# Kernel tuning notes

Hardware: AMD Instinct MI355X
Metric: run time of the kernel (lower is better)

The kernel has to match this reference:

```python
import jax, jax.numpy as jnp
import numpy as np

NUM_HEADS = 16

def setup_inputs() -> dict:
    key = jax.random.key(0)
    k1, k2, k3 = jax.random.split(key, 3)
    B, T, D = 4, 2048, 1024
    x = jax.random.normal(k1, (B, T, D), dtype=jnp.float32)
    # lecun_normal: std = 1/sqrt(fan_in)
    w = jax.random.normal(k2, (3 * D, D), dtype=jnp.float32) * (1.0 / np.sqrt(D))
    w_out = jax.random.normal(k3, (D, D), dtype=jnp.float32) * (1.0 / np.sqrt(D))
    return {"x": x, "w": w, "w_out": w_out}


def reference(x, w, w_out):
    B, T, D = x.shape
    H = NUM_HEADS
    L = D // H
    # qkv projection: (B,T,3D)
    q, k, v = jnp.split(jnp.matmul(x, w.T), 3, axis=2)
    # -> (T,B,H,L) time-major for the scan
    q = q.reshape(B, T, H, L).transpose(1, 0, 2, 3)
    k = k.reshape(B, T, H, L).transpose(1, 0, 2, 3)
    v = v.reshape(B, T, H, L).transpose(1, 0, 2, 3)
    scale = jax.lax.rsqrt(jnp.float32(L))
    k_exp = jnp.exp(k * scale) + 1e-6            # (T,B,H,L)
    k_norm = jnp.cumsum(k_exp, axis=0)           # causal normalizer
    qs = jax.nn.softmax(q * scale, axis=-1) / k_norm

    def step(carry, args):
        qs_t, k_t, v_t = args                    # each (B,H,L)
        # accumulate outer product k_t v_t^T into (B,H,L,L) state
        carry = carry + k_t[..., :, None] * v_t[..., None, :]
        y_t = jnp.einsum('bhl,bhlm->bhm', qs_t, carry)
        return carry, y_t

    init = jnp.zeros((B, H, L, L), dtype=x.dtype)
    _, y = jax.lax.scan(step, init, (qs, k_exp, v))   # y: (T,B,H,L)
    y = y.reshape(T, B, D).transpose(1, 0, 2)         # (B,T,D)
    return jnp.matmul(y, w_out)                       # Dense, no bias
```

## Files before the change

kernel.cpp:

```cpp
#include <hip/hip_runtime.h>
#include <math.h>

#define Bsz   4
#define Tsz   2048
#define Dsz   1024
#define Hsz   16
#define Lsz   64
#define BHsz  64
#define CH    64
#define NCH   32
#define QKVLD 3072
#define SCL   0.125f
#define QSC   512.0f
#define QSCI  (1.0f/512.0f)

typedef float  floatx4 __attribute__((ext_vector_type(4)));
typedef _Float16 half8 __attribute__((ext_vector_type(8)));
typedef _Float16 half4 __attribute__((ext_vector_type(4)));
typedef _Float16 half2v __attribute__((ext_vector_type(2)));

#define AS1 __attribute__((address_space(1)))
#define AS3 __attribute__((address_space(3)))

static __device__ __forceinline__ void gload_lds16(const void* g, void* l) {
  __builtin_amdgcn_global_load_lds((const AS1 unsigned int*)g,
                                   (AS3 unsigned int*)l, 16, 0, 0);
}

static __device__ __forceinline__ float wave_max64(float v) {
#pragma unroll
  for (int off = 1; off < 64; off <<= 1) v = fmaxf(v, __shfl_xor(v, off));
  return v;
}
static __device__ __forceinline__ float wave_sum64(float v) {
#pragma unroll
  for (int off = 1; off < 64; off <<= 1) v += __shfl_xor(v, off);
  return v;
}

__launch_bounds__(256)
__global__ void prep(const float* __restrict__ x, _Float16* __restrict__ xh,
                     const float* __restrict__ w, _Float16* __restrict__ wh,
                     const float* __restrict__ wo, _Float16* __restrict__ woT) {
  const int blk = blockIdx.x, tid = threadIdx.x;
  if (blk < 11264) {
    const float* in  = (blk < 8192) ? x : w;
    _Float16*   outp = (blk < 8192) ? xh : wh;
    const int bi = (blk < 8192) ? blk : blk - 8192;
    const int i = (bi * 256 + tid) * 4;
    float4 v = *(const float4*)(in + i);
    half4 h = { (_Float16)v.x, (_Float16)v.y, (_Float16)v.z, (_Float16)v.w };
    *(half4*)(outp + i) = h;
  } else {
    __shared__ float tile[32][33];
    const int bi = blk - 11264;
    const int bx = (bi & 31) * 32;
    const int by = (bi >> 5) * 32;
    const int tx = tid & 31, ty0 = tid >> 5;
#pragma unroll
    for (int p = 0; p < 4; p++) {
      const int ty = ty0 + p * 8;
      tile[ty][tx] = wo[(size_t)(by + ty) * 1024 + bx + tx];
    }
    __syncthreads();
#pragma unroll
    for (int p = 0; p < 4; p++) {
      const int ty = ty0 + p * 8;
      woT[(size_t)(bx + ty) * 1024 + by + tx] = (_Float16)tile[tx][ty];
    }
  }
}

__launch_bounds__(512, 2)
__global__ void qkv_gemm8(const _Float16* __restrict__ A, const _Float16* __restrict__ B,
                          _Float16* __restrict__ C) {
  __shared__ __align__(16) _Float16 AsF[2 * 256 * 64];
  __shared__ __align__(16) _Float16 BsF[2 * 256 * 64];
  const int tid  = threadIdx.x;
  const int wv   = tid >> 6, lane = tid & 63;
  const int wm   = wv >> 2, wn = wv & 3;
  const int fr   = lane & 15, fq = lane >> 4;

  const int flat = blockIdx.x;
  const int g  = (flat & 7) * 48 + (flat >> 3);
  const int m0 = (g / 12) * 256;
  const int n0 = (g % 12) * 256;

  const int srow = lane >> 3;
  const int scg  = (lane & 7) ^ srow;
  const int wv8  = wv * 8;
  const _Float16* aSrc = A + (size_t)(m0 + wv8 + srow) * 1024 + scg * 8;
  const _Float16* bSrc = B + (size_t)(n0 + wv8 + srow) * 1024 + scg * 8;

  const int sw  = fr & 7;
  const int ck0 = ((0 + fq) ^ sw) * 8;
  const int ck1 = ((4 + fq) ^ sw) * 8;
  const _Float16* apt = AsF + (wm * 64 + fr) * 64;
  const _Float16* bpt = BsF + (wn * 32 + fr) * 64;

  floatx4 acc[8][4];
#pragma unroll
  for (int i = 0; i < 8; i++)
#pragma unroll
    for (int j = 0; j < 4; j++) acc[i][j] = (floatx4){0.f, 0.f, 0.f, 0.f};

  half8 aF[8];
  half8 bF0[4], bF1[4];

#define BAR2() do { __builtin_amdgcn_s_barrier();                              \
                    asm volatile("" ::: "memory"); } while (0)
#define VMW4() asm volatile("s_waitcnt vmcnt(4)" ::: "memory")
#define SYNC() do { __builtin_amdgcn_s_barrier();                              \
    asm volatile("s_waitcnt lgkmcnt(0)" ::: "memory");                         \
    __builtin_amdgcn_sched_barrier(0); } while (0)

#define STAGE_A(kt, hm, sbuf) do {                                             \
    const _Float16* s_ = aSrc + (hm) * (128 * 1024) + (kt) * 64;               \
    gload_lds16(s_,             &AsF[(sbuf) * 16384 + ((hm) * 128 + wv8) * 64]);      \
    gload_lds16(s_ + 64 * 1024, &AsF[(sbuf) * 16384 + ((hm) * 128 + 64 + wv8) * 64]); \
  } while (0)
#define STAGE_B(kt, hm, sbuf) do {                                             \
    const _Float16* s_ = bSrc + (hm) * (128 * 1024) + (kt) * 64;               \
    gload_lds16(s_,             &BsF[(sbuf) * 16384 + ((hm) * 128 + wv8) * 64]);      \
    gload_lds16(s_ + 64 * 1024, &BsF[(sbuf) * 16384 + ((hm) * 128 + 64 + wv8) * 64]); \
  } while (0)

#define RD_A(buf, qm) do {                                                     \
    _Pragma("unroll")                                                          \
    for (int mf = 0; mf < 4; mf++) {                                           \
      const _Float16* p_ = apt + (buf) * 16384 + (qm) * 8192 + mf * 1024;      \
      aF[mf * 2]     = *(const half8*)(p_ + ck0);                              \
      aF[mf * 2 + 1] = *(const half8*)(p_ + ck1);                              \
    } } while (0)
#define RD_B(buf, qn, dst) do {                                                \
    _Pragma("unroll")                                                          \
    for (int nf = 0; nf < 2; nf++) {                                           \
      const _Float16* p_ = bpt + (buf) * 16384 + (qn) * 8192 + nf * 1024;      \
      dst[nf * 2]     = *(const half8*)(p_ + ck0);                             \
      dst[nf * 2 + 1] = *(const half8*)(p_ + ck1);                             \
    } } while (0)

#define MM(qm, qn, bb) do {                                                    \
    __builtin_amdgcn_s_setprio(1);                                             \
    _Pragma("unroll")                                                          \
    for (int mf = 0; mf < 4; mf++)                                             \
      _Pragma("unroll")                                                        \
      for (int nf = 0; nf < 2; nf++) {                                         \
        acc[(qm) * 4 + mf][(qn) * 2 + nf] = __builtin_amdgcn_mfma_f32_16x16x32_f16( \
            aF[mf * 2], bb[nf * 2], acc[(qm) * 4 + mf][(qn) * 2 + nf], 0, 0, 0);     \
        acc[(qm) * 4 + mf][(qn) * 2 + nf] = __builtin_amdgcn_mfma_f32_16x16x32_f16( \
            aF[mf * 2 + 1], bb[nf * 2 + 1], acc[(qm) * 4 + mf][(qn) * 2 + nf], 0, 0, 0); \
      }                                                                        \
    __builtin_amdgcn_s_setprio(0);                                             \
  } while (0)

  STAGE_A(0, 0, 0); STAGE_B(0, 0, 0); STAGE_A(0, 1, 0); STAGE_B(0, 1, 0);
  STAGE_A(1, 0, 1); STAGE_B(1, 0, 1);
  VMW4(); BAR2();

#pragma unroll 1
  for (int t = 0; t < 16; t += 2) {
    RD_A(0, 0); RD_B(0, 0, bF0); STAGE_A(t + 1, 1, 1);
    SYNC(); MM(0, 0, bF0); BAR2();

    RD_B(0, 1, bF1); STAGE_B(t + 1, 1, 1); STAGE_A(t + 2, 0, 0);
    SYNC(); MM(0, 1, bF1); BAR2();

    RD_A(0, 1); STAGE_B(t + 2, 0, 0);
    SYNC(); MM(1, 1, bF1); BAR2();

    VMW4();
    SYNC(); MM(1, 0, bF0); BAR2();

    RD_A(1, 0); RD_B(1, 0, bF0); STAGE_A(t + 2, 1, 0);
    SYNC(); MM(0, 0, bF0); BAR2();

    RD_B(1, 1, bF1); STAGE_B(t + 2, 1, 0); STAGE_A(t + 3, 0, 1);
    SYNC(); MM(0, 1, bF1); BAR2();

    RD_A(1, 1); STAGE_B(t + 3, 0, 1);
    SYNC(); MM(1, 1, bF1); BAR2();

    VMW4();
    SYNC(); MM(1, 0, bF0); BAR2();
  }

#undef MM
#undef RD_B
#undef RD_A
#undef STAGE_B
#undef STAGE_A
#undef SYNC
#undef VMW4
#undef BAR2

  const bool kreg = (n0 >= 1024) && (n0 < 2048);
#pragma unroll
  for (int qm = 0; qm < 2; qm++)
#pragma unroll
    for (int mf = 0; mf < 4; mf++) {
      const int row = m0 + qm * 128 + wm * 64 + mf * 16 + fq * 4;
#pragma unroll
      for (int qn = 0; qn < 2; qn++)
#pragma unroll
        for (int nf = 0; nf < 2; nf++) {
          const int col = n0 + qn * 128 + wn * 32 + nf * 16 + fr;
#pragma unroll
          for (int r = 0; r < 4; r++) {
            float v = acc[qm * 4 + mf][qn * 2 + nf][r];
            if (kreg) v = __expf(v * SCL) + 1e-6f;
            C[(size_t)(row + r) * 3072 + col] = (_Float16)v;
          }
        }
    }
}

__launch_bounds__(256)
__global__ void gemm_f16_bt_f32(const _Float16* __restrict__ A, const _Float16* __restrict__ B,
                                float* __restrict__ C, int M, int N, int K) {
  __shared__ _Float16 As[128][32];
  __shared__ _Float16 Bs[128][32];
  const int tid  = threadIdx.x;
  const int wave = tid >> 6, lane = tid & 63;
  const int flat = blockIdx.y * gridDim.x + blockIdx.x;
  const int xcd = flat & 7, g = flat >> 3;
  const int m0 = (xcd * 8 + (g & 7)) * 128;
  const int n0 = (g >> 3) * 128;
  const int wm = (wave >> 1) * 64, wn = (wave & 1) * 64;
  const int fr = lane & 15;
  const int fq = lane >> 4;
  const int lr = lane >> 2;
  const int lk = (lane & 3) * 8;

  floatx4 zero = {0.f, 0.f, 0.f, 0.f};
  floatx4 acc[4][4];
#pragma unroll
  for (int mt = 0; mt < 4; mt++)
#pragma unroll
    for (int nt = 0; nt < 4; nt++) acc[mt][nt] = zero;

  for (int k0 = 0; k0 < K; k0 += 32) {
    __syncthreads();
#pragma unroll
    for (int j = 0; j < 2; j++) {
      const int ia = wave * 2 + j;
      gload_lds16(A + (size_t)(m0 + ia * 16 + lr) * K + k0 + lk, &As[ia * 16][0]);
      gload_lds16(B + (size_t)(n0 + ia * 16 + lr) * K + k0 + lk, &Bs[ia * 16][0]);
    }
    __syncthreads();

    half8 af[4], bf[4];
#pragma unroll
    for (int i = 0; i < 4; i++) {
      af[i] = *(const half8*)&As[wm + i * 16 + fr][fq * 8];
      bf[i] = *(const half8*)&Bs[wn + i * 16 + fr][fq * 8];
    }
#pragma unroll
    for (int mt = 0; mt < 4; mt++)
#pragma unroll
      for (int nt = 0; nt < 4; nt++)
        acc[mt][nt] = __builtin_amdgcn_mfma_f32_16x16x32_f16(af[mt], bf[nt], acc[mt][nt], 0, 0, 0);
  }
#pragma unroll
  for (int mt = 0; mt < 4; mt++)
#pragma unroll
    for (int nt = 0; nt < 4; nt++)
#pragma unroll
      for (int r = 0; r < 4; r++) {
        const int row = m0 + wm + mt * 16 + fq * 4 + r;
        const int col = n0 + wn + nt * 16 + fr;
        C[(size_t)row * N + col] = acc[mt][nt][r];
      }
}

__launch_bounds__(256)
__global__ void chunk_kv(const _Float16* __restrict__ qkv, float* __restrict__ KV,
                         float* __restrict__ Ksum) {
  const int blk = blockIdx.x;
  const int bh = blk >> 3, cgrp = blk & 7;
  const int b = bh >> 4, h = bh & 15;
  const int tid = threadIdx.x;
  const int wave = tid >> 6, lane = tid & 63;
  const int fr = lane & 15, fq = lane >> 4;
  const int m2  = (tid & 31) * 2;
  const int tg8 = (tid >> 5) * 8;

  __shared__ __align__(16) _Float16 KxT[64][72];
  __shared__ __align__(16) _Float16 VT [64][72];

  for (int cc = 0; cc < 4; cc++) {
    const int c = cgrp * 4 + cc;
    const size_t base = ((size_t)(b * Tsz + c * CH)) * QKVLD + h * 64;
    __syncthreads();
    half8 klo, khi, vlo, vhi;
#pragma unroll
    for (int j = 0; j < 8; j++) {
      const int t = tg8 + j;
      half2v kk = *(const half2v*)(qkv + base + (size_t)t * QKVLD + 1024 + m2);
      klo[j] = kk[0]; khi[j] = kk[1];
      half2v vv = *(const half2v*)(qkv + base + (size_t)t * QKVLD + 2048 + m2);
      vlo[j] = vv[0]; vhi[j] = vv[1];
    }
    *(half8*)&KxT[m2][tg8]     = klo;
    *(half8*)&KxT[m2 + 1][tg8] = khi;
    *(half8*)&VT[m2][tg8]      = vlo;
    *(half8*)&VT[m2 + 1][tg8]  = vhi;
    __syncthreads();

    floatx4 acc[4];
#pragma unroll
    for (int j = 0; j < 4; j++) acc[j] = (floatx4){0.f, 0.f, 0.f, 0.f};
#pragma unroll
    for (int ks = 0; ks < 2; ks++) {
      half8 av = *(const half8*)&VT[wave * 16 + fr][ks * 32 + fq * 8];
#pragma unroll
      for (int j = 0; j < 4; j++) {
        half8 bv = *(const half8*)&KxT[j * 16 + fr][ks * 32 + fq * 8];
        acc[j] = __builtin_amdgcn_mfma_f32_16x16x32_f16(av, bv, acc[j], 0, 0, 0);
      }
    }
    float* KVp = KV + ((size_t)(bh * NCH + c)) * 4096;
#pragma unroll
    for (int j = 0; j < 4; j++)
#pragma unroll
      for (int r = 0; r < 4; r++)
        KVp[(wave * 16 + fq * 4 + r) * 64 + j * 16 + fr] = acc[j][r];

    if (tid < 64) {
      float s = 0.f;
      const half8* row = (const half8*)&KxT[tid][0];
#pragma unroll
      for (int j8 = 0; j8 < 8; j8++) {
        half8 v8 = row[j8];
#pragma unroll
        for (int j = 0; j < 8; j++) s += (float)v8[j];
      }
      Ksum[(bh * NCH + c) * 64 + tid] = s;
    }
  }
}

__launch_bounds__(256)
__global__ void prefix_kern(float* __restrict__ KV, float* __restrict__ Ksum) {
  const int tid = threadIdx.x;
  if (blockIdx.x < 256) {
    const int bh = blockIdx.x >> 2;
    const int e  = (blockIdx.x & 3) * 1024 + tid * 4;
    float4* p = (float4*)(KV + (size_t)bh * NCH * 4096 + e);
    float4 acc = {0.f, 0.f, 0.f, 0.f};
#pragma unroll 4
    for (int c = 0; c < NCH; c++) {
      float4 t = p[(size_t)c * 1024];
      p[(size_t)c * 1024] = acc;
      acc.x += t.x; acc.y += t.y; acc.z += t.z; acc.w += t.w;
    }
  } else {
    const int cid = (blockIdx.x - 256) * 256 + tid;
    const int bh = cid >> 4, l4 = cid & 15;
    float4* p = (float4*)(Ksum + (size_t)bh * NCH * 64) + l4;
    float4 acc = {0.f, 0.f, 0.f, 0.f};
#pragma unroll 4
    for (int c = 0; c < NCH; c++) {
      float4 t = p[c * 16];
      p[c * 16] = acc;
      acc.x += t.x; acc.y += t.y; acc.z += t.z; acc.w += t.w;
    }
  }
}

__launch_bounds__(256)
__global__ void chunk_y(const _Float16* __restrict__ qkv, const float* __restrict__ KV,
                        const float* __restrict__ Ksum, _Float16* __restrict__ Y) {
  const int bh = blockIdx.x, c = blockIdx.y;
  const int b = bh >> 4, h = bh & 15;
  const int tid = threadIdx.x;
  const int wave = tid >> 6, lane = tid & 63;
  const int fr = lane & 15, fq = lane >> 4;

  __shared__ __align__(16) _Float16 kxh[64][72];
  __shared__ __align__(16) _Float16 kxT[64][72];
  __shared__ __align__(16) _Float16 Ph[64][136];
  __shared__ __align__(16) _Float16 Bh[64][136];

  const size_t base = ((size_t)(b * Tsz + c * CH)) * QKVLD + h * 64;
  const float* KVp = KV + ((size_t)(bh * NCH + c)) * 4096;
  const int ksoff = (bh * NCH + c) * 64;

  _Float16 qreg[16];
#pragma unroll
  for (int i = 0; i < 16; i++)
    qreg[i] = qkv[base + (size_t)(wave * 16 + i) * QKVLD + lane];

  float ksb[4];
#pragma unroll
  for (int j = 0; j < 4; j++) ksb[j] = Ksum[ksoff + j * 16 + fr];

  {
    const int rr  = tid >> 3;
    const int sg8 = (tid & 7) * 8;
#pragma unroll
    for (int p = 0; p < 2; p++) {
      const int t = p * 32 + rr;
      *(half8*)&kxh[t][sg8] =
          *(const half8*)(qkv + base + (size_t)t * QKVLD + 1024 + sg8);
      *(half8*)&Ph[t][64 + sg8] =
          *(const half8*)(qkv + base + (size_t)t * QKVLD + 2048 + sg8);
    }
  }
  {
    const int m  = tid >> 2;
    const int l0 = (tid & 3) * 16;
#pragma unroll
    for (int q = 0; q < 2; q++) {
      float4 s0 = *(const float4*)(KVp + m * 64 + l0 + q * 8);
      float4 s1 = *(const float4*)(KVp + m * 64 + l0 + q * 8 + 4);
      half8 hh = { (_Float16)s0.x, (_Float16)s0.y, (_Float16)s0.z, (_Float16)s0.w,
                   (_Float16)s1.x, (_Float16)s1.y, (_Float16)s1.z, (_Float16)s1.w };
      *(half8*)&Bh[m][l0 + q * 8] = hh;
    }
  }
  __syncthreads();

  {
    const int l2  = (tid & 31) * 2;
    const int tg8 = (tid >> 5) * 8;
    half8 k0, k1, v0, v1;
#pragma unroll
    for (int j = 0; j < 8; j++) {
      const int t = tg8 + j;
      half2v kk = *(const half2v*)&kxh[t][l2];
      k0[j] = kk[0]; k1[j] = kk[1];
      half2v vv = *(const half2v*)&Ph[t][64 + l2];
      v0[j] = vv[0]; v1[j] = vv[1];
    }
    *(half8*)&kxT[l2][tg8]          = k0;
    *(half8*)&kxT[l2 + 1][tg8]      = k1;
    *(half8*)&Bh[l2][64 + tg8]      = v0;
    *(half8*)&Bh[l2 + 1][64 + tg8]  = v1;
  }
  __syncthreads();

  {
    floatx4 kacc[4];
#pragma unroll
    for (int j = 0; j < 4; j++) kacc[j] = (floatx4){0.f, 0.f, 0.f, 0.f};
#pragma unroll
    for (int ks = 0; ks < 2; ks++) {
      half8 af;
#pragma unroll
      for (int j = 0; j < 8; j++)
        af[j] = (ks * 32 + fq * 8 + j) <= (wave * 16 + fr) ? (_Float16)1.0f
                                                           : (_Float16)0.0f;
#pragma unroll
      for (int j = 0; j < 4; j++) {
        half8 bf = *(const half8*)&kxT[j * 16 + fr][ks * 32 + fq * 8];
        kacc[j] = __builtin_amdgcn_mfma_f32_16x16x32_f16(af, bf, kacc[j], 0, 0, 0);
      }
    }
    __syncthreads();
#pragma unroll
    for (int j = 0; j < 4; j++)
#pragma unroll
      for (int r = 0; r < 4; r++)
        kxT[wave * 16 + fq * 4 + r][j * 16 + fr] =
            (_Float16)(QSC / (ksb[j] + kacc[j][r]));
  }

#pragma unroll
  for (int i = 0; i < 16; i++) {
    const int t = wave * 16 + i;
    float v = (float)qreg[i] * SCL;
    float m = wave_max64(v);
    float e = __expf(v - m);
    float s = wave_sum64(e);
    Ph[t][lane] = (_Float16)((e / s) * (float)kxT[t][lane]);
  }
  __syncthreads();

  const int wm = (wave >> 1) * 32, wn = (wave & 1) * 32;
  {
    floatx4 a2[2][2];
#pragma unroll
    for (int mt = 0; mt < 2; mt++)
#pragma unroll
      for (int nt = 0; nt < 2; nt++) a2[mt][nt] = (floatx4){0.f, 0.f, 0.f, 0.f};
#pragma unroll
    for (int ks = 0; ks < 2; ks++) {
      half8 af[2], bf[2];
#pragma unroll
      for (int i = 0; i < 2; i++) {
        af[i] = *(const half8*)&Ph[wm + i * 16 + fr][ks * 32 + fq * 8];
        bf[i] = *(const half8*)&kxh[wn + i * 16 + fr][ks * 32 + fq * 8];
      }
#pragma unroll
      for (int mt = 0; mt < 2; mt++)
#pragma unroll
        for (int nt = 0; nt < 2; nt++)
          a2[mt][nt] = __builtin_amdgcn_mfma_f32_16x16x32_f16(af[mt], bf[nt], a2[mt][nt], 0, 0, 0);
    }
#pragma unroll
    for (int mt = 0; mt < 2; mt++)
#pragma unroll
      for (int nt = 0; nt < 2; nt++)
#pragma unroll
        for (int r = 0; r < 4; r++) {
          const int t = wm + mt * 16 + fq * 4 + r;
          const int s = wn + nt * 16 + fr;
          Ph[t][64 + s] = (_Float16)(s <= t ? a2[mt][nt][r] : 0.f);
        }
  }
  __syncthreads();

  {
    floatx4 acc[2][2];
#pragma unroll
    for (int mt = 0; mt < 2; mt++)
#pragma unroll
      for (int nt = 0; nt < 2; nt++) acc[mt][nt] = (floatx4){0.f, 0.f, 0.f, 0.f};
#pragma unroll
    for (int ks = 0; ks < 4; ks++) {
      half8 af[2], bf[2];
#pragma unroll
      for (int i = 0; i < 2; i++) {
        af[i] = *(const half8*)&Ph[wm + i * 16 + fr][ks * 32 + fq * 8];
        bf[i] = *(const half8*)&Bh[wn + i * 16 + fr][ks * 32 + fq * 8];
      }
#pragma unroll
      for (int mt = 0; mt < 2; mt++)
#pragma unroll
        for (int nt = 0; nt < 2; nt++)
          acc[mt][nt] = __builtin_amdgcn_mfma_f32_16x16x32_f16(af[mt], bf[nt], acc[mt][nt], 0, 0, 0);
    }
#pragma unroll
    for (int mt = 0; mt < 2; mt++)
#pragma unroll
      for (int nt = 0; nt < 2; nt++)
#pragma unroll
        for (int r = 0; r < 4; r++)
          kxh[wm + mt * 16 + fq * 4 + r][wn + nt * 16 + fr] =
              (_Float16)(acc[mt][nt][r] * QSCI);
  }
  __syncthreads();

  {
    const int ty = tid >> 2, sg = (tid & 3) * 16;
    _Float16* yrow = Y + (size_t)(b * Tsz + c * CH + ty) * Dsz + h * 64 + sg;
    *(half8*)(yrow)     = *(const half8*)&kxh[ty][sg];
    *(half8*)(yrow + 8) = *(const half8*)&kxh[ty][sg + 8];
  }
}

extern "C" void kernel_launch(void* const* d_in, const int* in_sizes, int n_in,
                              void* d_out, int out_size, void* d_ws, size_t ws_size,
                              hipStream_t stream) {
  const float* x     = (const float*)d_in[0];
  const float* w     = (const float*)d_in[1];
  const float* w_out = (const float*)d_in[2];
  float* out = (float*)d_out;

  _Float16* xh   = (_Float16*)d_ws;
  _Float16* Yh   = xh;
  _Float16* wh   = xh + (size_t)8192 * 1024;
  _Float16* woT  = wh + (size_t)3072 * 1024;
  _Float16* qkvh = woT + (size_t)1024 * 1024;
  float* KV   = (float*)(qkvh + (size_t)8192 * 3072);
  float* Ksum = KV + (size_t)BHsz * NCH * 4096;

  prep<<<12288, 256, 0, stream>>>(x, xh, w, wh, w_out, woT);

  qkv_gemm8<<<384, 512, 0, stream>>>(xh, wh, qkvh);

  chunk_kv<<<512, 256, 0, stream>>>(qkvh, KV, Ksum);
  prefix_kern<<<260, 256, 0, stream>>>(KV, Ksum);
  chunk_y<<<dim3(BHsz, NCH), 256, 0, stream>>>(qkvh, KV, Ksum, Yh);

  gemm_f16_bt_f32<<<dim3(8, 64), 256, 0, stream>>>(Yh, woT, out, 8192, 1024, 1024);
}
```

Before: 249.1 us.

## Fuse per-chunk KV state computation with the chunk prefix scan

```diff
diff --git a/kernel.cpp b/kernel.cpp
--- a/kernel.cpp
+++ b/kernel.cpp
@@ -274,98 +274,98 @@
 }
 
 __launch_bounds__(256)
-__global__ void chunk_kv(const _Float16* __restrict__ qkv, float* __restrict__ KV,
-                         float* __restrict__ Ksum) {
+__global__ void chunk_scan(const _Float16* __restrict__ qkv, float* __restrict__ KV,
+                           float* __restrict__ Ksum) {
   const int blk = blockIdx.x;
-  const int bh = blk >> 3, cgrp = blk & 7;
+  const int bh = blk >> 2, mq = blk & 3;
   const int b = bh >> 4, h = bh & 15;
   const int tid = threadIdx.x;
   const int wave = tid >> 6, lane = tid & 63;
   const int fr = lane & 15, fq = lane >> 4;
+
   const int m2  = (tid & 31) * 2;
   const int tg8 = (tid >> 5) * 8;
-
-  __shared__ __align__(16) _Float16 KxT[64][72];
-  __shared__ __align__(16) _Float16 VT [64][72];
-
-  for (int cc = 0; cc < 4; cc++) {
-    const int c = cgrp * 4 + cc;
-    const size_t base = ((size_t)(b * Tsz + c * CH)) * QKVLD + h * 64;
-    __syncthreads();
-    half8 klo, khi, vlo, vhi;
-#pragma unroll
-    for (int j = 0; j < 8; j++) {
-      const int t = tg8 + j;
-      half2v kk = *(const half2v*)(qkv + base + (size_t)t * QKVLD + 1024 + m2);
-      klo[j] = kk[0]; khi[j] = kk[1];
-      half2v vv = *(const half2v*)(qkv + base + (size_t)t * QKVLD + 2048 + m2);
-      vlo[j] = vv[0]; vhi[j] = vv[1];
-    }
-    *(half8*)&KxT[m2][tg8]     = klo;
-    *(half8*)&KxT[m2 + 1][tg8] = khi;
-    *(half8*)&VT[m2][tg8]      = vlo;
-    *(half8*)&VT[m2 + 1][tg8]  = vhi;
-    __syncthreads();
-
-    floatx4 acc[4];
-#pragma unroll
-    for (int j = 0; j < 4; j++) acc[j] = (floatx4){0.f, 0.f, 0.f, 0.f};
+  const int vcp2 = (tid & 7) * 2;
+  const int vtg8 = ((tid >> 3) & 7) * 8;
+
+  __shared__ __align__(16) _Float16 KxT[2][64][72];
+  __shared__ __align__(16) _Float16 VT [2][16][72];
+
+  const size_t bbase = ((size_t)b * Tsz) * QKVLD + h * 64;
+
+  half8 klo, khi, vlo, vhi;
+
+#define LOADC(c) do {                                                          \
+    const size_t base_ = bbase + (size_t)(c) * CH * QKVLD;                     \
+    _Pragma("unroll")                                                          \
+    for (int j = 0; j < 8; j++) {                                              \
+      half2v kk = *(const half2v*)(qkv + base_ + (size_t)(tg8 + j) * QKVLD + 1024 + m2); \
+      klo[j] = kk[0]; khi[j] = kk[1];                                          \
+    }                                                                          \
+    if (tid < 64) {                                                            \
+      _Pragma("unroll")                                                        \
+      for (int j = 0; j < 8; j++) {                                            \
+        half2v vv = *(const half2v*)(qkv + base_ + (size_t)(vtg8 + j) * QKVLD + 2048 + mq * 16 + vcp2); \
+        vlo[j] = vv[0]; vhi[j] = vv[1];                                        \
+      }                                                                        \
+    } } while (0)
+
+#define WRITEC(bufi) do {                                                      \
+    *(half8*)&KxT[bufi][m2][tg8]     = klo;                                    \
+    *(half8*)&KxT[bufi][m2 + 1][tg8] = khi;                                    \
+    if (tid < 64) {                                                            \
+      *(half8*)&VT[bufi][vcp2][vtg8]     = vlo;                                \
+      *(half8*)&VT[bufi][vcp2 + 1][vtg8] = vhi;                                \
+    } } while (0)
+
+  LOADC(0);
+  WRITEC(0);
+  __syncthreads();
+
+  floatx4 run = {0.f, 0.f, 0.f, 0.f};
+  float run_ks = 0.f;
+  int cur = 0;
+
+#pragma unroll 1
+  for (int c = 0; c < NCH; c++) {
+    if (c + 1 < NCH) LOADC(c + 1);
+
+    floatx4 acc = {0.f, 0.f, 0.f, 0.f};
 #pragma unroll
     for (int ks = 0; ks < 2; ks++) {
-      half8 av = *(const half8*)&VT[wave * 16 + fr][ks * 32 + fq * 8];
-#pragma unroll
-      for (int j = 0; j < 4; j++) {
-        half8 bv = *(const half8*)&KxT[j * 16 + fr][ks * 32 + fq * 8];
-        acc[j] = __builtin_amdgcn_mfma_f32_16x16x32_f16(av, bv, acc[j], 0, 0, 0);
-      }
-    }
+      half8 av = *(const half8*)&VT[cur][fr][ks * 32 + fq * 8];
+      half8 bv = *(const half8*)&KxT[cur][wave * 16 + fr][ks * 32 + fq * 8];
+      acc = __builtin_amdgcn_mfma_f32_16x16x32_f16(av, bv, acc, 0, 0, 0);
+    }
+
     float* KVp = KV + ((size_t)(bh * NCH + c)) * 4096;
 #pragma unroll
-    for (int j = 0; j < 4; j++)
-#pragma unroll
-      for (int r = 0; r < 4; r++)
-        KVp[(wave * 16 + fq * 4 + r) * 64 + j * 16 + fr] = acc[j][r];
-
-    if (tid < 64) {
+    for (int r = 0; r < 4; r++)
+      KVp[(mq * 16 + fq * 4 + r) * 64 + wave * 16 + fr] = run[r];
+    run = run + acc;
+
+    if (mq == 0 && tid < 64) {
       float s = 0.f;
-      const half8* row = (const half8*)&KxT[tid][0];
+      const half8* row = (const half8*)&KxT[cur][tid][0];
 #pragma unroll
       for (int j8 = 0; j8 < 8; j8++) {
         half8 v8 = row[j8];
 #pragma unroll
         for (int j = 0; j < 8; j++) s += (float)v8[j];
       }
-      Ksum[(bh * NCH + c) * 64 + tid] = s;
-    }
-  }
-}
-
-__launch_bounds__(256)
-__global__ void prefix_kern(float* __restrict__ KV, float* __restrict__ Ksum) {
-  const int tid = threadIdx.x;
-  if (blockIdx.x < 256) {
-    const int bh = blockIdx.x >> 2;
-    const int e  = (blockIdx.x & 3) * 1024 + tid * 4;
-    float4* p = (float4*)(KV + (size_t)bh * NCH * 4096 + e);
-    float4 acc = {0.f, 0.f, 0.f, 0.f};
-#pragma unroll 4
-    for (int c = 0; c < NCH; c++) {
-      float4 t = p[(size_t)c * 1024];
-      p[(size_t)c * 1024] = acc;
-      acc.x += t.x; acc.y += t.y; acc.z += t.z; acc.w += t.w;
-    }
-  } else {
-    const int cid = (blockIdx.x - 256) * 256 + tid;
-    const int bh = cid >> 4, l4 = cid & 15;
-    float4* p = (float4*)(Ksum + (size_t)bh * NCH * 64) + l4;
-    float4 acc = {0.f, 0.f, 0.f, 0.f};
-#pragma unroll 4
-    for (int c = 0; c < NCH; c++) {
-      float4 t = p[c * 16];
-      p[c * 16] = acc;
-      acc.x += t.x; acc.y += t.y; acc.z += t.z; acc.w += t.w;
-    }
-  }
+      Ksum[(bh * NCH + c) * 64 + tid] = run_ks;
+      run_ks += s;
+    }
+
+    if (c + 1 < NCH) {
+      WRITEC(cur ^ 1);
+      cur ^= 1;
+    }
+    __syncthreads();
+  }
+
+#undef WRITEC
+#undef LOADC
 }
 
 __launch_bounds__(256)
@@ -570,8 +570,7 @@
 
   qkv_gemm8<<<384, 512, 0, stream>>>(xh, wh, qkvh);
 
-  chunk_kv<<<512, 256, 0, stream>>>(qkvh, KV, Ksum);
-  prefix_kern<<<260, 256, 0, stream>>>(KV, Ksum);
+  chunk_scan<<<256, 256, 0, stream>>>(qkvh, KV, Ksum);
   chunk_y<<<dim3(BHsz, NCH), 256, 0, stream>>>(qkvh, KV, Ksum, Yh);
 
   gemm_f16_bt_f32<<<dim3(8, 64), 256, 0, stream>>>(Yh, woT, out, 8192, 1024, 1024);
```

Result: slower. 259.8 us (+4.3%).

## Simplify QKV GEMM to single-stage K=32 double-buffered loop without LDS swizzle

Applied to the files above, without the earlier changes.

```diff
diff --git a/kernel.cpp b/kernel.cpp
--- a/kernel.cpp
+++ b/kernel.cpp
@@ -71,11 +71,11 @@
   }
 }
 
-__launch_bounds__(512, 2)
-__global__ void qkv_gemm8(const _Float16* __restrict__ A, const _Float16* __restrict__ B,
-                          _Float16* __restrict__ C) {
-  __shared__ __align__(16) _Float16 AsF[2 * 256 * 64];
-  __shared__ __align__(16) _Float16 BsF[2 * 256 * 64];
+__launch_bounds__(512, 4)
+__global__ void qkv_gemm(const _Float16* __restrict__ A, const _Float16* __restrict__ B,
+                         _Float16* __restrict__ C) {
+  __shared__ __align__(16) _Float16 As[2][256][32];
+  __shared__ __align__(16) _Float16 Bs[2][256][32];
   const int tid  = threadIdx.x;
   const int wv   = tid >> 6, lane = tid & 63;
   const int wm   = wv >> 2, wn = wv & 3;
@@ -86,17 +86,15 @@
   const int m0 = (g / 12) * 256;
   const int n0 = (g % 12) * 256;
 
-  const int srow = lane >> 3;
-  const int scg  = (lane & 7) ^ srow;
-  const int wv8  = wv * 8;
-  const _Float16* aSrc = A + (size_t)(m0 + wv8 + srow) * 1024 + scg * 8;
-  const _Float16* bSrc = B + (size_t)(n0 + wv8 + srow) * 1024 + scg * 8;
-
-  const int sw  = fr & 7;
-  const int ck0 = ((0 + fq) ^ sw) * 8;
-  const int ck1 = ((4 + fq) ^ sw) * 8;
-  const _Float16* apt = AsF + (wm * 64 + fr) * 64;
-  const _Float16* bpt = BsF + (wn * 32 + fr) * 64;
+  const int srow = lane >> 2;
+  const int scg  = lane & 3;
+  const _Float16* aSrc = A + (size_t)(m0 + wv * 32 + srow) * 1024 + scg * 8;
+  const _Float16* bSrc = B + (size_t)(n0 + wv * 32 + srow) * 1024 + scg * 8;
+  _Float16* aBase = &As[0][0][0];
+  _Float16* bBase = &Bs[0][0][0];
+
+  const _Float16* apt = aBase + (wm * 128 + fr) * 32 + fq * 8;
+  const _Float16* bpt = bBase + (wn * 64 + fr) * 32 + fq * 8;
 
   floatx4 acc[8][4];
 #pragma unroll
@@ -104,8 +102,7 @@
 #pragma unroll
     for (int j = 0; j < 4; j++) acc[i][j] = (floatx4){0.f, 0.f, 0.f, 0.f};
 
-  half8 aF[8];
-  half8 bF0[4], bF1[4];
+  half8 aF[8], bF[4];
 
 #define BAR2() do { __builtin_amdgcn_s_barrier();                              \
                     asm volatile("" ::: "memory"); } while (0)
@@ -114,105 +111,76 @@
     asm volatile("s_waitcnt lgkmcnt(0)" ::: "memory");                         \
     __builtin_amdgcn_sched_barrier(0); } while (0)
 
-#define STAGE_A(kt, hm, sbuf) do {                                             \
-    const _Float16* s_ = aSrc + (hm) * (128 * 1024) + (kt) * 64;               \
-    gload_lds16(s_,             &AsF[(sbuf) * 16384 + ((hm) * 128 + wv8) * 64]);      \
-    gload_lds16(s_ + 64 * 1024, &AsF[(sbuf) * 16384 + ((hm) * 128 + 64 + wv8) * 64]); \
+#define STAGE_AB(kt, bufi) do {                                                \
+    const _Float16* sa_ = aSrc + (size_t)(kt) * 32;                            \
+    const _Float16* sb_ = bSrc + (size_t)(kt) * 32;                            \
+    gload_lds16(sa_,             aBase + (bufi) * 8192 + (wv * 32) * 32 + lane * 8);      \
+    gload_lds16(sa_ + 16 * 1024, aBase + (bufi) * 8192 + (wv * 32 + 16) * 32 + lane * 8); \
+    gload_lds16(sb_,             bBase + (bufi) * 8192 + (wv * 32) * 32 + lane * 8);      \
+    gload_lds16(sb_ + 16 * 1024, bBase + (bufi) * 8192 + (wv * 32 + 16) * 32 + lane * 8); \
   } while (0)
-#define STAGE_B(kt, hm, sbuf) do {                                             \
-    const _Float16* s_ = bSrc + (hm) * (128 * 1024) + (kt) * 64;               \
-    gload_lds16(s_,             &BsF[(sbuf) * 16384 + ((hm) * 128 + wv8) * 64]);      \
-    gload_lds16(s_ + 64 * 1024, &BsF[(sbuf) * 16384 + ((hm) * 128 + 64 + wv8) * 64]); \
+
+#define RD12(bufi) do {                                                        \
+    _Pragma("unroll")                                                          \
+    for (int mf = 0; mf < 8; mf++)                                             \
+      aF[mf] = *(const half8*)(apt + (bufi) * 8192 + mf * 512);                \
+    _Pragma("unroll")                                                          \
+    for (int nf = 0; nf < 4; nf++)                                             \
+      bF[nf] = *(const half8*)(bpt + (bufi) * 8192 + nf * 512);                \
   } while (0)
 
-#define RD_A(buf, qm) do {                                                     \
-    _Pragma("unroll")                                                          \
-    for (int mf = 0; mf < 4; mf++) {                                           \
-      const _Float16* p_ = apt + (buf) * 16384 + (qm) * 8192 + mf * 1024;      \
-      aF[mf * 2]     = *(const half8*)(p_ + ck0);                              \
-      aF[mf * 2 + 1] = *(const half8*)(p_ + ck1);                              \
-    } } while (0)
-#define RD_B(buf, qn, dst) do {                                                \
-    _Pragma("unroll")                                                          \
-    for (int nf = 0; nf < 2; nf++) {                                           \
-      const _Float16* p_ = bpt + (buf) * 16384 + (qn) * 8192 + nf * 1024;      \
-      dst[nf * 2]     = *(const half8*)(p_ + ck0);                             \
-      dst[nf * 2 + 1] = *(const half8*)(p_ + ck1);                             \
-    } } while (0)
-
-#define MM(qm, qn, bb) do {                                                    \
+#define MM32() do {                                                            \
     __builtin_amdgcn_s_setprio(1);                                             \
     _Pragma("unroll")                                                          \
-    for (int mf = 0; mf < 4; mf++)                                             \
+    for (int mf = 0; mf < 8; mf++)                                             \
       _Pragma("unroll")                                                        \
-      for (int nf = 0; nf < 2; nf++) {                                         \
-        acc[(qm) * 4 + mf][(qn) * 2 + nf] = __builtin_amdgcn_mfma_f32_16x16x32_f16( \
-            aF[mf * 2], bb[nf * 2], acc[(qm) * 4 + mf][(qn) * 2 + nf], 0, 0, 0);     \
-        acc[(qm) * 4 + mf][(qn) * 2 + nf] = __builtin_amdgcn_mfma_f32_16x16x32_f16( \
-            aF[mf * 2 + 1], bb[nf * 2 + 1], acc[(qm) * 4 + mf][(qn) * 2 + nf], 0, 0, 0); \
-      }                                                                        \
+      for (int nf = 0; nf < 4; nf++)                                           \
+        acc[mf][nf] = __builtin_amdgcn_mfma_f32_16x16x32_f16(aF[mf], bF[nf],   \
+                                                             acc[mf][nf], 0, 0, 0); \
     __builtin_amdgcn_s_setprio(0);                                             \
   } while (0)
 
-  STAGE_A(0, 0, 0); STAGE_B(0, 0, 0); STAGE_A(0, 1, 0); STAGE_B(0, 1, 0);
-  STAGE_A(1, 0, 1); STAGE_B(1, 0, 1);
+  STAGE_AB(0, 0);
+  STAGE_AB(1, 1);
   VMW4(); BAR2();
 
 #pragma unroll 1
-  for (int t = 0; t < 16; t += 2) {
-    RD_A(0, 0); RD_B(0, 0, bF0); STAGE_A(t + 1, 1, 1);
-    SYNC(); MM(0, 0, bF0); BAR2();
-
-    RD_B(0, 1, bF1); STAGE_B(t + 1, 1, 1); STAGE_A(t + 2, 0, 0);
-    SYNC(); MM(0, 1, bF1); BAR2();
-
-    RD_A(0, 1); STAGE_B(t + 2, 0, 0);
-    SYNC(); MM(1, 1, bF1); BAR2();
-
+  for (int t = 0; t < 32; t += 2) {
+    RD12(0);
+    SYNC(); MM32(); BAR2();
+    STAGE_AB(t + 2, 0);
     VMW4();
-    SYNC(); MM(1, 0, bF0); BAR2();
-
-    RD_A(1, 0); RD_B(1, 0, bF0); STAGE_A(t + 2, 1, 0);
-    SYNC(); MM(0, 0, bF0); BAR2();
-
-    RD_B(1, 1, bF1); STAGE_B(t + 2, 1, 0); STAGE_A(t + 3, 0, 1);
-    SYNC(); MM(0, 1, bF1); BAR2();
-
-    RD_A(1, 1); STAGE_B(t + 3, 0, 1);
-    SYNC(); MM(1, 1, bF1); BAR2();
-
+    BAR2();
+
+    RD12(1);
+    SYNC(); MM32(); BAR2();
+    STAGE_AB(t + 3, 1);
     VMW4();
-    SYNC(); MM(1, 0, bF0); BAR2();
-  }
-
-#undef MM
-#undef RD_B
-#undef RD_A
-#undef STAGE_B
-#undef STAGE_A
+    BAR2();
+  }
+
+#undef MM32
+#undef RD12
+#undef STAGE_AB
 #undef SYNC
 #undef VMW4
 #undef BAR2
 
   const bool kreg = (n0 >= 1024) && (n0 < 2048);
 #pragma unroll
-  for (int qm = 0; qm < 2; qm++)
-#pragma unroll
-    for (int mf = 0; mf < 4; mf++) {
-      const int row = m0 + qm * 128 + wm * 64 + mf * 16 + fq * 4;
-#pragma unroll
-      for (int qn = 0; qn < 2; qn++)
-#pragma unroll
-        for (int nf = 0; nf < 2; nf++) {
-          const int col = n0 + qn * 128 + wn * 32 + nf * 16 + fr;
-#pragma unroll
-          for (int r = 0; r < 4; r++) {
-            float v = acc[qm * 4 + mf][qn * 2 + nf][r];
-            if (kreg) v = __expf(v * SCL) + 1e-6f;
-            C[(size_t)(row + r) * 3072 + col] = (_Float16)v;
-          }
-        }
-    }
+  for (int mf = 0; mf < 8; mf++) {
+    const int row = m0 + wm * 128 + mf * 16 + fq * 4;
+#pragma unroll
+    for (int nf = 0; nf < 4; nf++) {
+      const int col = n0 + wn * 64 + nf * 16 + fr;
+#pragma unroll
+      for (int r = 0; r < 4; r++) {
+        float v = acc[mf][nf][r];
+        if (kreg) v = __expf(v * SCL) + 1e-6f;
+        C[(size_t)(row + r) * 3072 + col] = (_Float16)v;
+      }
+    }
+  }
 }
 
 __launch_bounds__(256)
@@ -568,7 +536,7 @@
 
   prep<<<12288, 256, 0, stream>>>(x, xh, w, wh, w_out, woT);
 
-  qkv_gemm8<<<384, 512, 0, stream>>>(xh, wh, qkvh);
+  qkv_gemm<<<384, 512, 0, stream>>>(xh, wh, qkvh);
 
   chunk_kv<<<512, 256, 0, stream>>>(qkvh, KV, Ksum);
   prefix_kern<<<260, 256, 0, stream>>>(KV, Ksum);
```

After: 788.1 us. +216.4%, slower.

## Double-buffer LDS in output-projection GEMM with async prefetch pipeline

Applied to the files above, without the earlier changes.

```diff
diff --git a/kernel.cpp b/kernel.cpp
--- a/kernel.cpp
+++ b/kernel.cpp
@@ -216,61 +216,111 @@
 }
 
 __launch_bounds__(256)
-__global__ void gemm_f16_bt_f32(const _Float16* __restrict__ A, const _Float16* __restrict__ B,
-                                float* __restrict__ C, int M, int N, int K) {
-  __shared__ _Float16 As[128][32];
-  __shared__ _Float16 Bs[128][32];
-  const int tid  = threadIdx.x;
-  const int wave = tid >> 6, lane = tid & 63;
-  const int flat = blockIdx.y * gridDim.x + blockIdx.x;
-  const int xcd = flat & 7, g = flat >> 3;
-  const int m0 = (xcd * 8 + (g & 7)) * 128;
-  const int n0 = (g >> 3) * 128;
-  const int wm = (wave >> 1) * 64, wn = (wave & 1) * 64;
-  const int fr = lane & 15;
-  const int fq = lane >> 4;
-  const int lr = lane >> 2;
-  const int lk = (lane & 3) * 8;
-
-  floatx4 zero = {0.f, 0.f, 0.f, 0.f};
+__global__ void gemm2(const _Float16* __restrict__ A, const _Float16* __restrict__ B,
+                      float* __restrict__ C) {
+  __shared__ __align__(16) _Float16 As[2][128][32];
+  __shared__ __align__(16) _Float16 Bs[2][128][32];
+  const int tid = threadIdx.x;
+  const int wv = tid >> 6, lane = tid & 63;
+  const int wm = wv >> 1, wn = wv & 1;
+  const int fr = lane & 15, fq = lane >> 4;
+
+  const int flat = blockIdx.x;
+  const int xcd = flat & 7, loc = flat >> 3;
+  const int m0 = (xcd * 8 + (loc >> 3)) * 128;
+  const int n0 = (loc & 7) * 128;
+
+  const int srow = lane >> 2;
+  const int scg  = lane & 3;
+  const _Float16* aSrc = A + (size_t)(m0 + wv * 32 + srow) * 1024 + scg * 8;
+  const _Float16* bSrc = B + (size_t)(n0 + wv * 32 + srow) * 1024 + scg * 8;
+  _Float16* aBase = &As[0][0][0];
+  _Float16* bBase = &Bs[0][0][0];
+
+  const _Float16* apt = aBase + (wm * 64 + fr) * 32 + fq * 8;
+  const _Float16* bpt = bBase + (wn * 64 + fr) * 32 + fq * 8;
+
   floatx4 acc[4][4];
 #pragma unroll
-  for (int mt = 0; mt < 4; mt++)
-#pragma unroll
-    for (int nt = 0; nt < 4; nt++) acc[mt][nt] = zero;
-
-  for (int k0 = 0; k0 < K; k0 += 32) {
-    __syncthreads();
-#pragma unroll
-    for (int j = 0; j < 2; j++) {
-      const int ia = wave * 2 + j;
-      gload_lds16(A + (size_t)(m0 + ia * 16 + lr) * K + k0 + lk, &As[ia * 16][0]);
-      gload_lds16(B + (size_t)(n0 + ia * 16 + lr) * K + k0 + lk, &Bs[ia * 16][0]);
-    }
-    __syncthreads();
-
-    half8 af[4], bf[4];
-#pragma unroll
-    for (int i = 0; i < 4; i++) {
-      af[i] = *(const half8*)&As[wm + i * 16 + fr][fq * 8];
-      bf[i] = *(const half8*)&Bs[wn + i * 16 + fr][fq * 8];
-    }
-#pragma unroll
-    for (int mt = 0; mt < 4; mt++)
-#pragma unroll
-      for (int nt = 0; nt < 4; nt++)
-        acc[mt][nt] = __builtin_amdgcn_mfma_f32_16x16x32_f16(af[mt], bf[nt], acc[mt][nt], 0, 0, 0);
-  }
-#pragma unroll
-  for (int mt = 0; mt < 4; mt++)
-#pragma unroll
-    for (int nt = 0; nt < 4; nt++)
-#pragma unroll
-      for (int r = 0; r < 4; r++) {
-        const int row = m0 + wm + mt * 16 + fq * 4 + r;
-        const int col = n0 + wn + nt * 16 + fr;
-        C[(size_t)row * N + col] = acc[mt][nt][r];
-      }
+  for (int i = 0; i < 4; i++)
+#pragma unroll
+    for (int j = 0; j < 4; j++) acc[i][j] = (floatx4){0.f, 0.f, 0.f, 0.f};
+
+  half8 aF[4], bF[4];
+
+#define BAR2() do { __builtin_amdgcn_s_barrier();                              \
+                    asm volatile("" ::: "memory"); } while (0)
+#define VMW4() asm volatile("s_waitcnt vmcnt(4)" ::: "memory")
+#define SYNC() do { __builtin_amdgcn_s_barrier();                              \
+    asm volatile("s_waitcnt lgkmcnt(0)" ::: "memory");                         \
+    __builtin_amdgcn_sched_barrier(0); } while (0)
+
+#define STAGE(kt, bufi) do {                                                   \
+    const _Float16* sa_ = aSrc + (size_t)(kt) * 32;                            \
+    const _Float16* sb_ = bSrc + (size_t)(kt) * 32;                            \
+    gload_lds16(sa_,             aBase + (bufi) * 4096 + (wv * 32) * 32 + lane * 8);      \
+    gload_lds16(sa_ + 16 * 1024, aBase + (bufi) * 4096 + (wv * 32 + 16) * 32 + lane * 8); \
+    gload_lds16(sb_,             bBase + (bufi) * 4096 + (wv * 32) * 32 + lane * 8);      \
+    gload_lds16(sb_ + 16 * 1024, bBase + (bufi) * 4096 + (wv * 32 + 16) * 32 + lane * 8); \
+  } while (0)
+
+#define RD8(bufi) do {                                                         \
+    _Pragma("unroll")                                                          \
+    for (int mf = 0; mf < 4; mf++)                                             \
+      aF[mf] = *(const half8*)(apt + (bufi) * 4096 + mf * 512);                \
+    _Pragma("unroll")                                                          \
+    for (int nf = 0; nf < 4; nf++)                                             \
+      bF[nf] = *(const half8*)(bpt + (bufi) * 4096 + nf * 512);                \
+  } while (0)
+
+#define MM16() do {                                                            \
+    __builtin_amdgcn_s_setprio(1);                                             \
+    _Pragma("unroll")                                                          \
+    for (int mt = 0; mt < 4; mt++)                                             \
+      _Pragma("unroll")                                                        \
+      for (int nt = 0; nt < 4; nt++)                                           \
+        acc[mt][nt] = __builtin_amdgcn_mfma_f32_16x16x32_f16(aF[mt], bF[nt],   \
+                                                             acc[mt][nt], 0, 0, 0); \
+    __builtin_amdgcn_s_setprio(0);                                             \
+  } while (0)
+
+  STAGE(0, 0);
+  STAGE(1, 1);
+  VMW4(); BAR2();
+
+#pragma unroll 1
+  for (int t = 0; t < 32; t += 2) {
+    RD8(0);
+    SYNC(); MM16(); BAR2();
+    STAGE(t + 2, 0);
+    VMW4();
+    BAR2();
+
+    RD8(1);
+    SYNC(); MM16(); BAR2();
+    STAGE(t + 3, 1);
+    VMW4();
+    BAR2();
+  }
+
+#undef MM16
+#undef RD8
+#undef STAGE
+#undef SYNC
+#undef VMW4
+#undef BAR2
+
+#pragma unroll
+  for (int mt = 0; mt < 4; mt++) {
+    const int row = m0 + wm * 64 + mt * 16 + fq * 4;
+#pragma unroll
+    for (int nt = 0; nt < 4; nt++) {
+      const int col = n0 + wn * 64 + nt * 16 + fr;
+#pragma unroll
+      for (int r = 0; r < 4; r++)
+        C[(size_t)(row + r) * 1024 + col] = acc[mt][nt][r];
+    }
+  }
 }
 
 __launch_bounds__(256)
@@ -574,5 +624,5 @@
   prefix_kern<<<260, 256, 0, stream>>>(KV, Ksum);
   chunk_y<<<dim3(BHsz, NCH), 256, 0, stream>>>(qkvh, KV, Ksum, Yh);
 
-  gemm_f16_bt_f32<<<dim3(8, 64), 256, 0, stream>>>(Yh, woT, out, 8192, 1024, 1024);
-}
+  gemm2<<<512, 256, 0, stream>>>(Yh, woT, out);
+}
```

Result: faster. 243.7 us (-2.2%).
